# Kernel tuning notes

Hardware: AMD Instinct MI355X
Metric: run time of the kernel (lower is better)

The kernel has to match this reference:

```python
import jax, jax.numpy as jnp
import numpy as np

EMBED_DIM = 1024
NUM_HEADS = 16
N = 32768


def setup_inputs() -> dict:
    key = jax.random.key(0)
    k1, k2, k3 = jax.random.split(key, 3)
    h = jax.random.normal(k1, (N, EMBED_DIM), dtype=jnp.float32)
    # torch nn.Linear(E, 3E): weight [3E, E], bias [3E] (bias=True by default)
    W_qkv = jax.random.normal(k2, (3 * EMBED_DIM, EMBED_DIM), dtype=jnp.float32) * 0.02
    b_qkv = jax.random.normal(k3, (3 * EMBED_DIM,), dtype=jnp.float32) * 0.02
    return {"h": h, "W_qkv": W_qkv, "b_qkv": b_qkv}


def reference(h, W_qkv, b_qkv):
    n, e = h.shape
    head_dim = e // NUM_HEADS
    # fused QKV projection: [N, 3E]
    qkv = h @ W_qkv.T + b_qkv
    # reshape [N, 3, H, D] -> split
    qkv = qkv.reshape(n, 3, NUM_HEADS, head_dim)
    q, k, v = qkv[:, 0], qkv[:, 1], qkv[:, 2]  # each [N, H, D]
    # NOTE: attention over the HEAD axis per token, scaled by sqrt(embed_dim)
    scores = jnp.einsum("nid,njd->nij", q, k) / (e ** 0.5)  # [N, H, H]
    attn = jax.nn.softmax(scores, axis=-1)
    out = jnp.einsum("nij,njd->nid", attn, v)  # [N, H, D]
    # faithful to torch: permute(1,0,2) then reshape(N, E) (mixes node order)
    out = jnp.transpose(out, (1, 0, 2)).reshape(n, e)
    return out
```

## Files before the change

kernel.cpp:

```cpp
#include <hip/hip_runtime.h>
#include <stdint.h>

#define NTOK 32768
#define EMB  1024
#define QKVN 3072
#define NH   16
#define HD   64

typedef __bf16 bf16x8 __attribute__((ext_vector_type(8)));
typedef float  floatx4 __attribute__((ext_vector_type(4)));
typedef unsigned int   uintx4   __attribute__((ext_vector_type(4)));
typedef unsigned short ushortx4 __attribute__((ext_vector_type(4)));
typedef unsigned short ushortx8 __attribute__((ext_vector_type(8)));

__device__ __forceinline__ unsigned short f2bf_rne(float f){
    unsigned int x; __builtin_memcpy(&x, &f, 4);
    x += 0x7fffu + ((x >> 16) & 1u);
    return (unsigned short)(x >> 16);
}

__device__ __forceinline__ void async_copy16(void* lds, const void* gsrc){
    __builtin_amdgcn_global_load_lds(
        (const __attribute__((address_space(1))) unsigned int*)gsrc,
        (__attribute__((address_space(3))) unsigned int*)lds,
        16, 0, 0);
}

__global__ __launch_bounds__(256) void cast_f32_bf16(const float* __restrict__ in,
                                                     unsigned short* __restrict__ out,
                                                     int n4){
    int idx = blockIdx.x * 256 + threadIdx.x;
    if (idx < n4){
        floatx4 v = ((const floatx4*)in)[idx];
        ushortx4 o;
        o[0] = f2bf_rne(v[0]); o[1] = f2bf_rne(v[1]);
        o[2] = f2bf_rne(v[2]); o[3] = f2bf_rne(v[3]);
        ((ushortx4*)out)[idx] = o;
    }
}


__device__ __forceinline__ void stage_a_q(unsigned short* At, const unsigned short* A,
                                          int m0, int q, int kt, int tid){
    int g     = tid >> 8;
    int rl    = (tid & 255) >> 3;
    int chunk = tid & 7;
    int row   = g * 128 + q * 32 + rl;
    int k8    = chunk ^ (row & 7);
    async_copy16((char*)At + row * 128 + chunk * 16,
                 &A[(size_t)(m0 + row) * EMB + kt + k8 * 8]);
}

__device__ __forceinline__ void stage_b_half(unsigned short* Bt, const unsigned short* B,
                                             int n0, int h, int kt, int tid){
    #pragma unroll
    for (int j = 0; j < 2; j++){
        int qg    = j * 2 + (tid >> 8);
        int row0  = qg * 64 + h * 32;
        int t2    = tid & 255;
        int rl    = t2 >> 3;
        int chunk = tid & 7;
        int row   = row0 + rl;
        int k8    = chunk ^ (row & 7);
        async_copy16((char*)Bt + row0 * 128 + t2 * 16,
                     &B[(size_t)(n0 + row) * EMB + kt + k8 * 8]);
    }
}

#define LDA_Q(DST, BUF, Q)                                                          \
    _Pragma("unroll")                                                               \
    for (int mi = 0; mi < 2; mi++){                                                 \
        int row = wm * 128 + (Q) * 32 + mi * 16 + r16;                              \
        _Pragma("unroll")                                                           \
        for (int ks = 0; ks < 2; ks++)                                              \
            DST[mi][ks] = *(const bf16x8*)&(BUF)[row * 64 + (((quad + 4*ks) ^ (row & 7)) * 8)]; \
    }

#define LDB_P(DST, BUF, P)                                                          \
    _Pragma("unroll")                                                               \
    for (int ni = 0; ni < 2; ni++){                                                 \
        int row = wn * 64 + (P) * 32 + ni * 16 + r16;                               \
        _Pragma("unroll")                                                           \
        for (int ks = 0; ks < 2; ks++)                                              \
            DST[ni][ks] = *(const bf16x8*)&(BUF)[row * 64 + (((quad + 4*ks) ^ (row & 7)) * 8)]; \
    }

#define MFMA8(Q, P, AS, BS)                                                         \
    _Pragma("unroll")                                                               \
    for (int mi = 0; mi < 2; mi++)                                                  \
        _Pragma("unroll")                                                           \
        for (int ni = 0; ni < 2; ni++)                                              \
            _Pragma("unroll")                                                       \
            for (int ks = 0; ks < 2; ks++)                                          \
                acc[(Q)*2 + mi][(P)*2 + ni] = __builtin_amdgcn_mfma_f32_16x16x32_bf16( \
                    AS[mi][ks], BS[ni][ks], acc[(Q)*2 + mi][(P)*2 + ni], 0, 0, 0);

#define SETP1 __builtin_amdgcn_s_setprio(1)
#define SETP0 __builtin_amdgcn_s_setprio(0)
#define BAR   __builtin_amdgcn_s_barrier()

__device__ __forceinline__ void ktile8(const unsigned short* __restrict__ A,
                                       const unsigned short* __restrict__ B,
                                       unsigned short* curA, unsigned short* curB,
                                       unsigned short* nxtA, unsigned short* nxtB,
                                       int m0, int n0, int kt, int tid,
                                       bf16x8 (&aX)[2][2], bf16x8 (&aY)[2][2],
                                       bf16x8 (&b01)[2][2], bf16x8 (&b23)[2][2],
                                       floatx4 (&acc)[8][4]){
    const int lane = tid & 63;
    const int wave = tid >> 6;
    const int wm = wave >> 2, wn = wave & 3;
    const int r16 = lane & 15, quad = lane >> 4;
    const int ks2 = kt + 128;

    SETP1; MFMA8(0, 0, aX, b01); SETP0; BAR;

    LDA_Q(aY, curA, 1);
    stage_a_q(curA, A, m0, 0, ks2, tid);
    stage_b_half(curB, B, n0, 0, ks2, tid);
    SETP1; MFMA8(0, 1, aX, b23); SETP0; BAR;

    stage_b_half(curB, B, n0, 1, ks2, tid);
    SETP1; MFMA8(1, 1, aY, b23); SETP0; BAR;

    LDA_Q(aX, curA, 2);
    stage_a_q(curA, A, m0, 1, ks2, tid);
    SETP1; MFMA8(1, 0, aY, b01); SETP0; BAR;

    SETP1; MFMA8(2, 0, aX, b01); SETP0; BAR;

    LDA_Q(aY, curA, 3);
    stage_a_q(curA, A, m0, 2, ks2, tid);
    SETP1; MFMA8(2, 1, aX, b23); SETP0; BAR;

    SETP1; MFMA8(3, 1, aY, b23); SETP0;
    asm volatile("s_waitcnt vmcnt(7)" ::: "memory");
    BAR;

    LDB_P(b23, nxtB, 1);
    LDA_Q(aX, nxtA, 0);
    SETP1; MFMA8(3, 0, aY, b01); SETP0;
    LDB_P(b01, nxtB, 0);
    stage_a_q(curA, A, m0, 3, ks2, tid);
    BAR;
}

__global__ __launch_bounds__(512, 2) void qkv_gemm256(const unsigned short* __restrict__ A,
                                                      const unsigned short* __restrict__ B,
                                                      const float* __restrict__ bias,
                                                      unsigned short* __restrict__ C){
    extern __shared__ __align__(16) unsigned short lds[];
    unsigned short* A0 = lds;
    unsigned short* B0 = lds + 16384;
    unsigned short* A1 = lds + 32768;
    unsigned short* B1 = lds + 49152;

    const int tid = threadIdx.x;
    int bid = blockIdx.x;
    int swz = (bid & 7) * 192 + (bid >> 3);
    int by  = swz / 12;
    int bx  = swz - by * 12;
    const int m0 = by * 256, n0 = bx * 256;

    const int lane = tid & 63;
    const int wave = tid >> 6;
    const int wm = wave >> 2, wn = wave & 3;
    const int r16 = lane & 15, quad = lane >> 4;

    floatx4 acc[8][4];
    #pragma unroll
    for (int i = 0; i < 8; i++)
        #pragma unroll
        for (int j = 0; j < 4; j++) acc[i][j] = floatx4{0.f, 0.f, 0.f, 0.f};

    #pragma unroll
    for (int q = 0; q < 4; q++) stage_a_q(A0, A, m0, q, 0, tid);
    stage_b_half(B0, B, n0, 0, 0, tid);
    stage_b_half(B0, B, n0, 1, 0, tid);
    #pragma unroll
    for (int q = 0; q < 4; q++) stage_a_q(A1, A, m0, q, 64, tid);
    stage_b_half(B1, B, n0, 0, 64, tid);
    stage_b_half(B1, B, n0, 1, 64, tid);
    asm volatile("s_waitcnt vmcnt(8)" ::: "memory");
    BAR;

    bf16x8 aX[2][2], aY[2][2], b01[2][2], b23[2][2];
    LDA_Q(aX, A0, 0);
    LDB_P(b01, B0, 0);
    LDB_P(b23, B0, 1);

    #pragma unroll 1
    for (int t = 0; t < 16; t += 2){
        ktile8(A, B, A0, B0, A1, B1, m0, n0, t * 64,      tid, aX, aY, b01, b23, acc);
        ktile8(A, B, A1, B1, A0, B0, m0, n0, t * 64 + 64, tid, aX, aY, b01, b23, acc);
    }

    #pragma unroll
    for (int ni = 0; ni < 4; ni++){
        int gcol = n0 + wn * 64 + ni * 16 + r16;
        float bv = bias[gcol];
        #pragma unroll
        for (int mi = 0; mi < 8; mi++){
            #pragma unroll
            for (int r = 0; r < 4; r++){
                int grow = m0 + wm * 128 + mi * 16 + quad * 4 + r;
                C[(size_t)grow * QKVN + gcol] = f2bf_rne(acc[mi][ni][r] + bv);
            }
        }
    }
}

#define TOKL 3072
#define KOFF 0
#define VOFF 1152
#define POFF 2688

__global__ __launch_bounds__(256) void attn_mfma(const unsigned short* __restrict__ qkv,
                                                 float* __restrict__ out){
    __shared__ unsigned short sm[4 * TOKL];

    const int tid = threadIdx.x;
    const int n0  = blockIdx.x * 4;

    #pragma unroll
    for (int s = 0; s < 2; s++){
        int c   = tid + s * 256;
        int t   = c >> 7;
        int rem = c & 127;
        int j   = rem >> 3;
        int d8  = (rem & 7) * 8;
        ushortx8 kk = *(const ushortx8*)&qkv[(size_t)(n0 + t) * QKVN + EMB + j * HD + d8];
        *(ushortx8*)&sm[t * TOKL + KOFF + j * 72 + d8] = kk;
        ushortx8 vv = *(const ushortx8*)&qkv[(size_t)(n0 + t) * QKVN + 2 * EMB + j * HD + d8];
        #pragma unroll
        for (int e = 0; e < 8; e++)
            sm[t * TOKL + VOFF + (d8 + e) * 24 + j] = vv[e];
    }
    __syncthreads();

    const int wave = tid >> 6;
    const int lane = tid & 63;
    const int col  = lane & 15;
    const int quad = lane >> 4;
    const int n    = n0 + wave;
    unsigned short* tb = &sm[wave * TOKL];

    const unsigned short* qrow = qkv + (size_t)n * QKVN + col * HD;
    bf16x8 qf0 = *(const bf16x8*)(qrow + quad * 8);
    bf16x8 qf1 = *(const bf16x8*)(qrow + 32 + quad * 8);
    bf16x8 kf0 = *(const bf16x8*)&tb[KOFF + col * 72 + quad * 8];
    bf16x8 kf1 = *(const bf16x8*)&tb[KOFF + col * 72 + 32 + quad * 8];

    floatx4 sAcc = floatx4{0.f, 0.f, 0.f, 0.f};
    sAcc = __builtin_amdgcn_mfma_f32_16x16x32_bf16(qf0, kf0, sAcc, 0, 0, 0);
    sAcc = __builtin_amdgcn_mfma_f32_16x16x32_bf16(qf1, kf1, sAcc, 0, 0, 0);

    #pragma unroll
    for (int r = 0; r < 4; r++){
        float sv = sAcc[r] * 0.03125f;
        float m = sv;
        m = fmaxf(m, __shfl_xor(m, 1));
        m = fmaxf(m, __shfl_xor(m, 2));
        m = fmaxf(m, __shfl_xor(m, 4));
        m = fmaxf(m, __shfl_xor(m, 8));
        float p = __expf(sv - m);
        float l = p;
        l += __shfl_xor(l, 1);
        l += __shfl_xor(l, 2);
        l += __shfl_xor(l, 4);
        l += __shfl_xor(l, 8);
        p *= 1.f / l;
        tb[POFF + (quad * 4 + r) * 24 + col] = f2bf_rne(p);
    }

    bf16x8 pf;
    #pragma unroll
    for (int z = 0; z < 8; z++) pf[z] = (__bf16)0.0f;
    if (quad < 2) pf = *(const bf16x8*)&tb[POFF + col * 24 + quad * 8];

    #pragma unroll
    for (int dblk = 0; dblk < 4; dblk++){
        bf16x8 vf;
        #pragma unroll
        for (int z = 0; z < 8; z++) vf[z] = (__bf16)0.0f;
        if (quad < 2) vf = *(const bf16x8*)&tb[VOFF + (dblk * 16 + col) * 24 + quad * 8];
        floatx4 o = __builtin_amdgcn_mfma_f32_16x16x32_bf16(
                        pf, vf, floatx4{0.f, 0.f, 0.f, 0.f}, 0, 0, 0);
        #pragma unroll
        for (int r = 0; r < 4; r++){
            int i = quad * 4 + r;
            out[(size_t)i * (NTOK * HD) + (size_t)n * HD + dblk * 16 + col] = o[r];
        }
    }
}

extern "C" void kernel_launch(void* const* d_in, const int* in_sizes, int n_in,
                              void* d_out, int out_size, void* d_ws, size_t ws_size,
                              hipStream_t stream){
    const float* h = (const float*)d_in[0];
    const float* W = (const float*)d_in[1];
    const float* b = (const float*)d_in[2];
    float* out = (float*)d_out;

    char* ws = (char*)d_ws;
    unsigned short* h_bf = (unsigned short*)ws;
    unsigned short* w_bf = (unsigned short*)(ws + (size_t)64 * 1024 * 1024);
    unsigned short* qkv  = (unsigned short*)(ws + (size_t)72 * 1024 * 1024);

    static bool attr_set = false;
    if (!attr_set){
        hipFuncSetAttribute(reinterpret_cast<const void*>(qkv_gemm256),
                            hipFuncAttributeMaxDynamicSharedMemorySize, 131072);
        attr_set = true;
    }

    cast_f32_bf16<<<(NTOK * EMB / 4 + 255) / 256, 256, 0, stream>>>(h, h_bf, NTOK * EMB / 4);
    cast_f32_bf16<<<(QKVN * EMB / 4 + 255) / 256, 256, 0, stream>>>(W, w_bf, QKVN * EMB / 4);

    qkv_gemm256<<<dim3(1536), 512, 131072, stream>>>(h_bf, w_bf, b, qkv);

    attn_mfma<<<NTOK / 4, 256, 0, stream>>>(qkv, out);
}
```

Before: 511.5 us.

## Pre-transpose V in GEMM epilogue, split GEMM launch, multi-group attention loop

The GEMM epilogue now writes the V section of the QKV buffer head-transposed (d-major), so the attention kernel can stage V into shared memory with vector stores instead of scalar transposing stores. The GEMM is split into two launches over column halves with an adjusted tile swizzle. The attention kernel now processes four token groups per block and software-pipelines the global loads for the next group behind the current group's compute, with a raised occupancy hint. The GEMM epilogue gains a strided scatter for V columns, and there is an extra launch plus an extra barrier per iteration.

```diff
diff --git a/kernel.cpp b/kernel.cpp
--- a/kernel.cpp
+++ b/kernel.cpp
@@ -148,7 +148,8 @@
 __global__ __launch_bounds__(512, 2) void qkv_gemm256(const unsigned short* __restrict__ A,
                                                       const unsigned short* __restrict__ B,
                                                       const float* __restrict__ bias,
-                                                      unsigned short* __restrict__ C){
+                                                      unsigned short* __restrict__ C,
+                                                      int n_off){
     extern __shared__ __align__(16) unsigned short lds[];
     unsigned short* A0 = lds;
     unsigned short* B0 = lds + 16384;
@@ -157,10 +158,10 @@
 
     const int tid = threadIdx.x;
     int bid = blockIdx.x;
-    int swz = (bid & 7) * 192 + (bid >> 3);
-    int by  = swz / 12;
-    int bx  = swz - by * 12;
-    const int m0 = by * 256, n0 = bx * 256;
+    int swz = (bid & 7) * 96 + (bid >> 3);
+    int by  = swz / 6;
+    int bx  = swz - by * 6;
+    const int m0 = by * 256, n0 = n_off + bx * 256;
 
     const int lane = tid & 63;
     const int wave = tid >> 6;
@@ -199,12 +200,17 @@
     for (int ni = 0; ni < 4; ni++){
         int gcol = n0 + wn * 64 + ni * 16 + r16;
         float bv = bias[gcol];
+        int pcol = gcol;
+        if (gcol >= 2048){
+            int off = gcol - 2048;
+            pcol = 2048 + ((off & 63) << 4) + (off >> 6);
+        }
         #pragma unroll
         for (int mi = 0; mi < 8; mi++){
             #pragma unroll
             for (int r = 0; r < 4; r++){
                 int grow = m0 + wm * 128 + mi * 16 + quad * 4 + r;
-                C[(size_t)grow * QKVN + gcol] = f2bf_rne(acc[mi][ni][r] + bv);
+                C[(size_t)grow * QKVN + pcol] = f2bf_rne(acc[mi][ni][r] + bv);
             }
         }
     }
@@ -215,82 +221,100 @@
 #define VOFF 1152
 #define POFF 2688
 
-__global__ __launch_bounds__(256) void attn_mfma(const unsigned short* __restrict__ qkv,
-                                                 float* __restrict__ out){
+__device__ __forceinline__ void attn_issue(const unsigned short* __restrict__ qkv,
+                                           int g, int tid, int wave, int col, int quad,
+                                           ushortx8 (&kk)[2], ushortx8 (&vv)[2],
+                                           bf16x8& qf0, bf16x8& qf1){
+    #pragma unroll
+    for (int s = 0; s < 2; s++){
+        int c = tid + s * 256, t = c >> 7, rem = c & 127;
+        const unsigned short* base = qkv + (size_t)(g * 4 + t) * QKVN;
+        kk[s] = *(const ushortx8*)(base + EMB   + (rem >> 3) * HD + (rem & 7) * 8);
+        vv[s] = *(const ushortx8*)(base + 2*EMB + (rem >> 1) * 16 + (rem & 1) * 8);
+    }
+    const unsigned short* qrow = qkv + (size_t)(g * 4 + wave) * QKVN + col * HD;
+    qf0 = *(const bf16x8*)(qrow + quad * 8);
+    qf1 = *(const bf16x8*)(qrow + 32 + quad * 8);
+}
+
+__global__ __launch_bounds__(256, 5) void attn_mfma(const unsigned short* __restrict__ qkv,
+                                                    float* __restrict__ out){
     __shared__ unsigned short sm[4 * TOKL];
 
-    const int tid = threadIdx.x;
-    const int n0  = blockIdx.x * 4;
-
-    #pragma unroll
-    for (int s = 0; s < 2; s++){
-        int c   = tid + s * 256;
-        int t   = c >> 7;
-        int rem = c & 127;
-        int j   = rem >> 3;
-        int d8  = (rem & 7) * 8;
-        ushortx8 kk = *(const ushortx8*)&qkv[(size_t)(n0 + t) * QKVN + EMB + j * HD + d8];
-        *(ushortx8*)&sm[t * TOKL + KOFF + j * 72 + d8] = kk;
-        ushortx8 vv = *(const ushortx8*)&qkv[(size_t)(n0 + t) * QKVN + 2 * EMB + j * HD + d8];
-        #pragma unroll
-        for (int e = 0; e < 8; e++)
-            sm[t * TOKL + VOFF + (d8 + e) * 24 + j] = vv[e];
-    }
-    __syncthreads();
-
+    const int tid  = threadIdx.x;
     const int wave = tid >> 6;
     const int lane = tid & 63;
     const int col  = lane & 15;
     const int quad = lane >> 4;
-    const int n    = n0 + wave;
-    unsigned short* tb = &sm[wave * TOKL];
-
-    const unsigned short* qrow = qkv + (size_t)n * QKVN + col * HD;
-    bf16x8 qf0 = *(const bf16x8*)(qrow + quad * 8);
-    bf16x8 qf1 = *(const bf16x8*)(qrow + 32 + quad * 8);
-    bf16x8 kf0 = *(const bf16x8*)&tb[KOFF + col * 72 + quad * 8];
-    bf16x8 kf1 = *(const bf16x8*)&tb[KOFF + col * 72 + 32 + quad * 8];
-
-    floatx4 sAcc = floatx4{0.f, 0.f, 0.f, 0.f};
-    sAcc = __builtin_amdgcn_mfma_f32_16x16x32_bf16(qf0, kf0, sAcc, 0, 0, 0);
-    sAcc = __builtin_amdgcn_mfma_f32_16x16x32_bf16(qf1, kf1, sAcc, 0, 0, 0);
-
-    #pragma unroll
-    for (int r = 0; r < 4; r++){
-        float sv = sAcc[r] * 0.03125f;
-        float m = sv;
-        m = fmaxf(m, __shfl_xor(m, 1));
-        m = fmaxf(m, __shfl_xor(m, 2));
-        m = fmaxf(m, __shfl_xor(m, 4));
-        m = fmaxf(m, __shfl_xor(m, 8));
-        float p = __expf(sv - m);
-        float l = p;
-        l += __shfl_xor(l, 1);
-        l += __shfl_xor(l, 2);
-        l += __shfl_xor(l, 4);
-        l += __shfl_xor(l, 8);
-        p *= 1.f / l;
-        tb[POFF + (quad * 4 + r) * 24 + col] = f2bf_rne(p);
-    }
-
-    bf16x8 pf;
-    #pragma unroll
-    for (int z = 0; z < 8; z++) pf[z] = (__bf16)0.0f;
-    if (quad < 2) pf = *(const bf16x8*)&tb[POFF + col * 24 + quad * 8];
-
-    #pragma unroll
-    for (int dblk = 0; dblk < 4; dblk++){
-        bf16x8 vf;
-        #pragma unroll
-        for (int z = 0; z < 8; z++) vf[z] = (__bf16)0.0f;
-        if (quad < 2) vf = *(const bf16x8*)&tb[VOFF + (dblk * 16 + col) * 24 + quad * 8];
-        floatx4 o = __builtin_amdgcn_mfma_f32_16x16x32_bf16(
-                        pf, vf, floatx4{0.f, 0.f, 0.f, 0.f}, 0, 0, 0);
+
+    const int g0 = blockIdx.x * 4;
+    ushortx8 kk[2], vv[2];
+    bf16x8 qf0, qf1;
+    attn_issue(qkv, g0, tid, wave, col, quad, kk, vv, qf0, qf1);
+
+    #pragma unroll 1
+    for (int it = 0; it < 4; it++){
+        const int g = g0 + it;
+
+        #pragma unroll
+        for (int s = 0; s < 2; s++){
+            int c = tid + s * 256, t = c >> 7, rem = c & 127;
+            *(ushortx8*)&sm[t * TOKL + KOFF + (rem >> 3) * 72 + (rem & 7) * 8] = kk[s];
+            *(ushortx8*)&sm[t * TOKL + VOFF + (rem >> 1) * 24 + (rem & 1) * 8] = vv[s];
+        }
+        __syncthreads();
+
+        bf16x8 q0 = qf0, q1 = qf1;
+        int gn = (it < 3) ? g + 1 : g;
+        attn_issue(qkv, gn, tid, wave, col, quad, kk, vv, qf0, qf1);
+
+        const int n = g * 4 + wave;
+        unsigned short* tb = &sm[wave * TOKL];
+
+        bf16x8 kf0 = *(const bf16x8*)&tb[KOFF + col * 72 + quad * 8];
+        bf16x8 kf1 = *(const bf16x8*)&tb[KOFF + col * 72 + 32 + quad * 8];
+        floatx4 sAcc = floatx4{0.f, 0.f, 0.f, 0.f};
+        sAcc = __builtin_amdgcn_mfma_f32_16x16x32_bf16(q0, kf0, sAcc, 0, 0, 0);
+        sAcc = __builtin_amdgcn_mfma_f32_16x16x32_bf16(q1, kf1, sAcc, 0, 0, 0);
+
         #pragma unroll
         for (int r = 0; r < 4; r++){
-            int i = quad * 4 + r;
-            out[(size_t)i * (NTOK * HD) + (size_t)n * HD + dblk * 16 + col] = o[r];
-        }
+            float sv = sAcc[r] * 0.03125f;
+            float m = sv;
+            m = fmaxf(m, __shfl_xor(m, 1));
+            m = fmaxf(m, __shfl_xor(m, 2));
+            m = fmaxf(m, __shfl_xor(m, 4));
+            m = fmaxf(m, __shfl_xor(m, 8));
+            float p = __expf(sv - m);
+            float l = p;
+            l += __shfl_xor(l, 1);
+            l += __shfl_xor(l, 2);
+            l += __shfl_xor(l, 4);
+            l += __shfl_xor(l, 8);
+            p *= 1.f / l;
+            tb[POFF + (quad * 4 + r) * 24 + col] = f2bf_rne(p);
+        }
+
+        bf16x8 pf;
+        #pragma unroll
+        for (int z = 0; z < 8; z++) pf[z] = (__bf16)0.0f;
+        if (quad < 2) pf = *(const bf16x8*)&tb[POFF + col * 24 + quad * 8];
+
+        #pragma unroll
+        for (int dblk = 0; dblk < 4; dblk++){
+            bf16x8 vf;
+            #pragma unroll
+            for (int z = 0; z < 8; z++) vf[z] = (__bf16)0.0f;
+            if (quad < 2) vf = *(const bf16x8*)&tb[VOFF + (dblk * 16 + col) * 24 + quad * 8];
+            floatx4 o = __builtin_amdgcn_mfma_f32_16x16x32_bf16(
+                            pf, vf, floatx4{0.f, 0.f, 0.f, 0.f}, 0, 0, 0);
+            #pragma unroll
+            for (int r = 0; r < 4; r++){
+                int i = quad * 4 + r;
+                out[(size_t)i * (NTOK * HD) + (size_t)n * HD + dblk * 16 + col] = o[r];
+            }
+        }
+        __syncthreads();
     }
 }
 
@@ -317,7 +341,8 @@
     cast_f32_bf16<<<(NTOK * EMB / 4 + 255) / 256, 256, 0, stream>>>(h, h_bf, NTOK * EMB / 4);
     cast_f32_bf16<<<(QKVN * EMB / 4 + 255) / 256, 256, 0, stream>>>(W, w_bf, QKVN * EMB / 4);
 
-    qkv_gemm256<<<dim3(1536), 512, 131072, stream>>>(h_bf, w_bf, b, qkv);
-
-    attn_mfma<<<NTOK / 4, 256, 0, stream>>>(qkv, out);
-}
+    qkv_gemm256<<<dim3(768), 512, 131072, stream>>>(h_bf, w_bf, b, qkv, 0);
+    qkv_gemm256<<<dim3(768), 512, 131072, stream>>>(h_bf, w_bf, b, qkv, 1536);
+
+    attn_mfma<<<NTOK / 16, 256, 0, stream>>>(qkv, out);
+}
```

New measurement: 580.6 us. +13.5%, slower.
